# Performance work log

Measured on AMD Instinct MI355X. Metric: run time of the kernel, lower is better.

Reference implementation:

```python
import jax, jax.numpy as jnp
import numpy as np

SEQ_LEN, LABEL_LEN, B = 256, 128, 8192
NF, NO, H = 8, 8, 64


def setup_inputs() -> dict:
    key = jax.random.key(0)
    ks = jax.random.split(key, 12)
    s = 1.0 / np.sqrt(H)  # PyTorch GRU init scale
    u = lambda k, shape: jax.random.uniform(k, shape, jnp.float32, -s, s)
    return {
        "x": jax.random.normal(ks[0], (SEQ_LEN, B, NF), jnp.float32),
        "xy": jax.random.normal(ks[1], (LABEL_LEN, B, NO), jnp.float32),
        "enc_Wih": u(ks[2], (3 * H, NF)),
        "enc_Whh": u(ks[3], (3 * H, H)),
        "enc_bih": u(ks[4], (3 * H,)),
        "enc_bhh": u(ks[5], (3 * H,)),
        "dec_Wih": u(ks[6], (3 * H, NO)),
        "dec_Whh": u(ks[7], (3 * H, H)),
        "dec_bih": u(ks[8], (3 * H,)),
        "dec_bhh": u(ks[9], (3 * H,)),
        "Wout": u(ks[10], (NO, H)),
        "bout": u(ks[11], (NO,)),
    }


def _gru_cell(h, xt, Wih, Whh, bih, bhh):
    # PyTorch GRU gate order: r, z, n
    gi = xt @ Wih.T + bih          # [B, 3H]
    gh = h @ Whh.T + bhh           # [B, 3H]
    ir, iz, inn = jnp.split(gi, 3, axis=-1)
    hr, hz, hn = jnp.split(gh, 3, axis=-1)
    r = jax.nn.sigmoid(ir + hr)
    z = jax.nn.sigmoid(iz + hz)
    n = jnp.tanh(inn + r * hn)
    return (1.0 - z) * n + z * h


def reference(x, xy, enc_Wih, enc_Whh, enc_bih, enc_bhh,
              dec_Wih, dec_Whh, dec_bih, dec_bhh, Wout, bout):
    batch = x.shape[1]
    hidden = enc_Whh.shape[1]
    h0 = jnp.zeros((batch, hidden), x.dtype)

    # Encoder: scan over seq_len, keep final hidden state
    def enc_step(h, xt):
        return _gru_cell(h, xt, enc_Wih, enc_Whh, enc_bih, enc_bhh), None
    h_enc, _ = jax.lax.scan(enc_step, h0, x)

    def dec_step(carry, _):
        inp, h = carry
        h = _gru_cell(h, inp, dec_Wih, dec_Whh, dec_bih, dec_bhh)
        out = h @ Wout.T + bout    # [B, NO]
        return (out, h), out

    (_, _), outputs = jax.lax.scan(dec_step, (xy[0], h_enc), None,
                                   length=xy.shape[0])
    return outputs  # [label_len, B, n_output]
```

## Files before the change

kernel.cpp:

```cpp
#include <hip/hip_runtime.h>


#define SEQ_LEN   256
#define LABEL_LEN 128
#define BATCH     8192
#define NF        8
#define NO        8
#define H         64

#define BB 16
#define HP 68
#define NBLOCKS (BATCH / BB)

__device__ __forceinline__ float sigmoid_f(float x) {
    float t = __expf(-x);
    return __fdividef(1.0f, 1.0f + t);
}

__device__ __forceinline__ float tanh_f(float x) {
    float ax = fabsf(x);
    float t = __expf(-2.0f * ax);
    float y = __fdividef(1.0f - t, 1.0f + t);
    return copysignf(y, x);
}

__device__ __forceinline__ void gru_cell(
    const float4 inp[8],
    const float* __restrict__ hc,
    float*       __restrict__ hn_,
    const float (&wr)[32], const float (&wz)[32], const float (&wn)[32],
    const float (&wxr)[4], const float (&wxz)[4], const float (&wxn)[4],
    float br, float bz, float bin, float bhn,
    int g, int j, int kh, int kbase)
{
    #pragma unroll
    for (int m = 0; m < 8; ++m) {
        const int bl = 8 * g + m;
        const float* hrow = hc + bl * HP + kbase;
        float aR = 0.0f, aZ = 0.0f, aNh = 0.0f, aNi = 0.0f;
        #pragma unroll
        for (int c = 0; c < 8; ++c) {
            const float4 hv = *reinterpret_cast<const float4*>(hrow + 4 * c);
            aR  = fmaf(hv.x, wr[4*c+0], aR);
            aR  = fmaf(hv.y, wr[4*c+1], aR);
            aR  = fmaf(hv.z, wr[4*c+2], aR);
            aR  = fmaf(hv.w, wr[4*c+3], aR);
            aZ  = fmaf(hv.x, wz[4*c+0], aZ);
            aZ  = fmaf(hv.y, wz[4*c+1], aZ);
            aZ  = fmaf(hv.z, wz[4*c+2], aZ);
            aZ  = fmaf(hv.w, wz[4*c+3], aZ);
            aNh = fmaf(hv.x, wn[4*c+0], aNh);
            aNh = fmaf(hv.y, wn[4*c+1], aNh);
            aNh = fmaf(hv.z, wn[4*c+2], aNh);
            aNh = fmaf(hv.w, wn[4*c+3], aNh);
        }
        const float4 xi = inp[m];
        aR  = fmaf(xi.x, wxr[0], aR);
        aR  = fmaf(xi.y, wxr[1], aR);
        aR  = fmaf(xi.z, wxr[2], aR);
        aR  = fmaf(xi.w, wxr[3], aR);
        aZ  = fmaf(xi.x, wxz[0], aZ);
        aZ  = fmaf(xi.y, wxz[1], aZ);
        aZ  = fmaf(xi.z, wxz[2], aZ);
        aZ  = fmaf(xi.w, wxz[3], aZ);
        aNi = fmaf(xi.x, wxn[0], aNi);
        aNi = fmaf(xi.y, wxn[1], aNi);
        aNi = fmaf(xi.z, wxn[2], aNi);
        aNi = fmaf(xi.w, wxn[3], aNi);

        aR  += __shfl_xor(aR,  32);
        aZ  += __shfl_xor(aZ,  32);
        aNh += __shfl_xor(aNh, 32);
        aNi += __shfl_xor(aNi, 32);

        const float r  = sigmoid_f(aR + br);
        const float z  = sigmoid_f(aZ + bz);
        const float nn = tanh_f(aNi + bin + r * (aNh + bhn));
        const float hold = hc[bl * HP + j];
        const float hv_  = (1.0f - z) * nn + z * hold;
        if (kh == 0) hn_[bl * HP + j] = hv_;
    }
}

#define LOAD_WEIGHTS(Wih_, Whh_, bih_, bhh_) do {                              \
    _Pragma("unroll")                                                          \
    for (int k = 0; k < 32; ++k) {                                             \
        wr[k] = Whh_[(        j) * H + kbase + k];                             \
        wz[k] = Whh_[( H   +  j) * H + kbase + k];                             \
        wn[k] = Whh_[( 2*H +  j) * H + kbase + k];                             \
    }                                                                          \
    _Pragma("unroll")                                                          \
    for (int i = 0; i < 4; ++i) {                                              \
        wxr[i] = Wih_[(        j) * NF + 4 * kh + i];                          \
        wxz[i] = Wih_[( H   +  j) * NF + 4 * kh + i];                          \
        wxn[i] = Wih_[( 2*H +  j) * NF + 4 * kh + i];                          \
    }                                                                          \
    br  = bih_[j]       + bhh_[j];                                             \
    bz  = bih_[H + j]   + bhh_[H + j];                                         \
    bin = bih_[2*H + j];                                                       \
    bhn = bhh_[2*H + j];                                                       \
} while (0)

__global__ __launch_bounds__(256, 2) void seq2seq_gru_kernel(
    const float* __restrict__ x,    const float* __restrict__ xy,
    const float* __restrict__ eWih, const float* __restrict__ eWhh,
    const float* __restrict__ ebih, const float* __restrict__ ebhh,
    const float* __restrict__ dWih, const float* __restrict__ dWhh,
    const float* __restrict__ dbih, const float* __restrict__ dbhh,
    const float* __restrict__ Wout, const float* __restrict__ bout,
    float* __restrict__ out)
{
    __shared__ __align__(16) float hbufA[BB * HP];
    __shared__ __align__(16) float hbufB[BB * HP];
    __shared__ __align__(16) float out_lds[BB * NO];
    __shared__ __align__(16) float wout_lds[NO * HP];

    const int tid   = threadIdx.x;
    const int lane  = tid & 63;
    const int wv    = tid >> 6;
    const int jj    = lane & 31;
    const int kh    = lane >> 5;
    const int jh    = wv & 1;
    const int g     = wv >> 1;
    const int j     = 32 * jh + jj;
    const int kbase = 32 * kh;
    const int b0    = (int)blockIdx.x * BB;

    for (int i = tid; i < BB * HP; i += 256) hbufA[i] = 0.0f;
    for (int i = tid; i < NO * H; i += 256) {
        const int o = i >> 6, k = i & 63;
        wout_lds[o * HP + k] = Wout[i];
    }
    const float bo = bout[lane & 7];

    float wr[32], wz[32], wn[32], wxr[4], wxz[4], wxn[4];
    float br, bz, bin, bhn;
    LOAD_WEIGHTS(eWih, eWhh, ebih, ebhh);

    __syncthreads();

    float* hc  = hbufA;
    float* hn_ = hbufB;

    for (int t = 0; t < SEQ_LEN; ++t) {
        float4 inp[8];
        const float* xrow = x + ((size_t)t * BATCH + (b0 + 8 * g)) * NF + 4 * kh;
        #pragma unroll
        for (int m = 0; m < 8; ++m)
            inp[m] = *reinterpret_cast<const float4*>(xrow + m * NF);
        gru_cell(inp, hc, hn_, wr, wz, wn, wxr, wxz, wxn, br, bz, bin, bhn,
                 g, j, kh, kbase);
        __syncthreads();
        float* tmp = hc; hc = hn_; hn_ = tmp;
    }

    LOAD_WEIGHTS(dWih, dWhh, dbih, dbhh);

    for (int d = 0; d < LABEL_LEN; ++d) {
        float4 inp[8];
        if (d == 0) {
            const float* xyrow = xy + (size_t)(b0 + 8 * g) * NO + 4 * kh;
            #pragma unroll
            for (int m = 0; m < 8; ++m)
                inp[m] = *reinterpret_cast<const float4*>(xyrow + m * NO);
        } else {
            #pragma unroll
            for (int m = 0; m < 8; ++m)
                inp[m] = *reinterpret_cast<const float4*>(
                    &out_lds[(8 * g + m) * NO + 4 * kh]);
        }
        gru_cell(inp, hc, hn_, wr, wz, wn, wxr, wxz, wxn, br, bz, bin, bhn,
                 g, j, kh, kbase);
        __syncthreads();

        {
            const int ob = lane >> 3;
            const int oo = lane & 7;
            const float* hrow = hn_ + (8 * g + ob) * HP;
            const float* wrow = wout_lds + oo * HP;
            float acc = bo;
            #pragma unroll
            for (int c = 0; c < 16; ++c) {
                const float4 hv = *reinterpret_cast<const float4*>(hrow + 4 * c);
                const float4 wv4 = *reinterpret_cast<const float4*>(wrow + 4 * c);
                acc = fmaf(hv.x, wv4.x, acc);
                acc = fmaf(hv.y, wv4.y, acc);
                acc = fmaf(hv.z, wv4.z, acc);
                acc = fmaf(hv.w, wv4.w, acc);
            }
            if (jh == 0) {
                out_lds[(8 * g + ob) * NO + oo] = acc;
                out[(size_t)d * (BATCH * NO) + (size_t)(b0 + 8 * g + ob) * NO + oo] = acc;
            }
        }
        __syncthreads();
        float* tmp = hc; hc = hn_; hn_ = tmp;
    }
}

extern "C" void kernel_launch(void* const* d_in, const int* in_sizes, int n_in,
                              void* d_out, int out_size, void* d_ws, size_t ws_size,
                              hipStream_t stream) {
    const float* x    = (const float*)d_in[0];
    const float* xy   = (const float*)d_in[1];
    const float* eWih = (const float*)d_in[2];
    const float* eWhh = (const float*)d_in[3];
    const float* ebih = (const float*)d_in[4];
    const float* ebhh = (const float*)d_in[5];
    const float* dWih = (const float*)d_in[6];
    const float* dWhh = (const float*)d_in[7];
    const float* dbih = (const float*)d_in[8];
    const float* dbhh = (const float*)d_in[9];
    const float* Wout = (const float*)d_in[10];
    const float* bout = (const float*)d_in[11];
    float* out = (float*)d_out;

    seq2seq_gru_kernel<<<NBLOCKS, 256, 0, stream>>>(
        x, xy, eWih, eWhh, ebih, ebhh, dWih, dWhh, dbih, dbhh, Wout, bout, out);
}
```

Baseline: 2.093 ms.

## Halve batch per block, keep own hidden state in registers, raise occupancy

Reduces the batch tile per block from 16 to 8 rows (4 rows per wave group), doubling the block count, and raises launch bounds to 4 blocks per CU. Each thread now keeps its own hidden element in registers instead of re-reading it from LDS, and only one wave computes the output projection. This aims to get more parallel blocks for latency hiding on a serial recurrence. The cost is that the per-thread weight registers (about 100 floats) are now amortized over fewer rows, and register pressure at the higher occupancy target may cause spills.

```diff
diff --git a/kernel.cpp b/kernel.cpp
--- a/kernel.cpp
+++ b/kernel.cpp
@@ -8,8 +8,9 @@
 #define NO        8
 #define H         64
 
-#define BB 16
-#define HP 68
+#define BB  8
+#define MPG 4
+#define HP  68
 #define NBLOCKS (BATCH / BB)
 
 __device__ __forceinline__ float sigmoid_f(float x) {
@@ -25,17 +26,18 @@
 }
 
 __device__ __forceinline__ void gru_cell(
-    const float4 inp[8],
+    const float4 inp[MPG],
     const float* __restrict__ hc,
     float*       __restrict__ hn_,
+    float (&hreg)[MPG],
     const float (&wr)[32], const float (&wz)[32], const float (&wn)[32],
     const float (&wxr)[4], const float (&wxz)[4], const float (&wxn)[4],
     float br, float bz, float bin, float bhn,
     int g, int j, int kh, int kbase)
 {
     #pragma unroll
-    for (int m = 0; m < 8; ++m) {
-        const int bl = 8 * g + m;
+    for (int m = 0; m < MPG; ++m) {
+        const int bl = MPG * g + m;
         const float* hrow = hc + bl * HP + kbase;
         float aR = 0.0f, aZ = 0.0f, aNh = 0.0f, aNi = 0.0f;
         #pragma unroll
@@ -76,8 +78,9 @@
         const float r  = sigmoid_f(aR + br);
         const float z  = sigmoid_f(aZ + bz);
         const float nn = tanh_f(aNi + bin + r * (aNh + bhn));
-        const float hold = hc[bl * HP + j];
+        const float hold = hreg[m];
         const float hv_  = (1.0f - z) * nn + z * hold;
+        hreg[m] = hv_;
         if (kh == 0) hn_[bl * HP + j] = hv_;
     }
 }
@@ -101,7 +104,7 @@
     bhn = bhh_[2*H + j];                                                       \
 } while (0)
 
-__global__ __launch_bounds__(256, 2) void seq2seq_gru_kernel(
+__global__ __launch_bounds__(256, 4) void seq2seq_gru_kernel(
     const float* __restrict__ x,    const float* __restrict__ xy,
     const float* __restrict__ eWih, const float* __restrict__ eWhh,
     const float* __restrict__ ebih, const float* __restrict__ ebhh,
@@ -137,18 +140,22 @@
     float br, bz, bin, bhn;
     LOAD_WEIGHTS(eWih, eWhh, ebih, ebhh);
 
+    float hreg[MPG];
+    #pragma unroll
+    for (int m = 0; m < MPG; ++m) hreg[m] = 0.0f;
+
     __syncthreads();
 
     float* hc  = hbufA;
     float* hn_ = hbufB;
 
     for (int t = 0; t < SEQ_LEN; ++t) {
-        float4 inp[8];
-        const float* xrow = x + ((size_t)t * BATCH + (b0 + 8 * g)) * NF + 4 * kh;
+        float4 inp[MPG];
+        const float* xrow = x + ((size_t)t * BATCH + (b0 + MPG * g)) * NF + 4 * kh;
         #pragma unroll
-        for (int m = 0; m < 8; ++m)
+        for (int m = 0; m < MPG; ++m)
             inp[m] = *reinterpret_cast<const float4*>(xrow + m * NF);
-        gru_cell(inp, hc, hn_, wr, wz, wn, wxr, wxz, wxn, br, bz, bin, bhn,
+        gru_cell(inp, hc, hn_, hreg, wr, wz, wn, wxr, wxz, wxn, br, bz, bin, bhn,
                  g, j, kh, kbase);
         __syncthreads();
         float* tmp = hc; hc = hn_; hn_ = tmp;
@@ -157,41 +164,39 @@
     LOAD_WEIGHTS(dWih, dWhh, dbih, dbhh);
 
     for (int d = 0; d < LABEL_LEN; ++d) {
-        float4 inp[8];
+        float4 inp[MPG];
         if (d == 0) {
-            const float* xyrow = xy + (size_t)(b0 + 8 * g) * NO + 4 * kh;
+            const float* xyrow = xy + (size_t)(b0 + MPG * g) * NO + 4 * kh;
             #pragma unroll
-            for (int m = 0; m < 8; ++m)
+            for (int m = 0; m < MPG; ++m)
                 inp[m] = *reinterpret_cast<const float4*>(xyrow + m * NO);
         } else {
             #pragma unroll
-            for (int m = 0; m < 8; ++m)
+            for (int m = 0; m < MPG; ++m)
                 inp[m] = *reinterpret_cast<const float4*>(
-                    &out_lds[(8 * g + m) * NO + 4 * kh]);
+                    &out_lds[(MPG * g + m) * NO + 4 * kh]);
         }
-        gru_cell(inp, hc, hn_, wr, wz, wn, wxr, wxz, wxn, br, bz, bin, bhn,
+        gru_cell(inp, hc, hn_, hreg, wr, wz, wn, wxr, wxz, wxn, br, bz, bin, bhn,
                  g, j, kh, kbase);
         __syncthreads();
 
-        {
+        if (wv == 0) {
             const int ob = lane >> 3;
             const int oo = lane & 7;
-            const float* hrow = hn_ + (8 * g + ob) * HP;
+            const float* hrow = hn_ + ob * HP;
             const float* wrow = wout_lds + oo * HP;
             float acc = bo;
             #pragma unroll
             for (int c = 0; c < 16; ++c) {
-                const float4 hv = *reinterpret_cast<const float4*>(hrow + 4 * c);
+                const float4 hv  = *reinterpret_cast<const float4*>(hrow + 4 * c);
                 const float4 wv4 = *reinterpret_cast<const float4*>(wrow + 4 * c);
                 acc = fmaf(hv.x, wv4.x, acc);
                 acc = fmaf(hv.y, wv4.y, acc);
                 acc = fmaf(hv.z, wv4.z, acc);
                 acc = fmaf(hv.w, wv4.w, acc);
             }
-            if (jh == 0) {
-                out_lds[(8 * g + ob) * NO + oo] = acc;
-                out[(size_t)d * (BATCH * NO) + (size_t)(b0 + 8 * g + ob) * NO + oo] = acc;
-            }
+            out_lds[(ob) * NO + oo] = acc;
+            out[(size_t)d * (BATCH * NO) + (size_t)(b0 + ob) * NO + oo] = acc;
         }
         __syncthreads();
         float* tmp = hc; hc = hn_; hn_ = tmp;
```

Measured after the change: 3.585 ms. 1.71x slower.
